# Optimization experiments

Measured on AMD Instinct MI355X. Metric: run time of the kernel, lower is better.

## Reference

```python
import jax, jax.numpy as jnp
import numpy as np

C = 128
NUM_GROUPS = 32
EPS = 1e-6


def setup_inputs() -> dict:
    key = jax.random.key(0)
    ks = jax.random.split(key, 6)
    B, H, W = 8, 64, 64
    x = jax.random.normal(ks[0], (B, C, H, W), dtype=jnp.float32)
    # 1x1 conv weights stored as [out_c, in_c] (kernel spatial dims are 1)
    fan_avg = C  # fan_in == fan_out == C for 1x1 conv
    bound = np.sqrt(3.0 / fan_avg)
    wq = jax.random.uniform(ks[1], (C, C), jnp.float32, -bound, bound)
    wk = jax.random.uniform(ks[2], (C, C), jnp.float32, -bound, bound)
    wv = jax.random.uniform(ks[3], (C, C), jnp.float32, -bound, bound)
    # proj_out has init_scale=0.0 -> near-zero init; use tiny random instead to test math
    wo = jax.random.uniform(ks[4], (C, C), jnp.float32, -bound, bound) * 1e-3
    bq = jnp.zeros((C,), jnp.float32)
    bk = jnp.zeros((C,), jnp.float32)
    bv = jnp.zeros((C,), jnp.float32)
    bo = jnp.zeros((C,), jnp.float32)
    gamma = jnp.ones((C,), jnp.float32)
    beta = jnp.zeros((C,), jnp.float32)
    return {"x": x, "gamma": gamma, "beta": beta,
            "wq": wq, "bq": bq, "wk": wk, "bk": bk,
            "wv": wv, "bv": bv, "wo": wo, "bo": bo}


def _group_norm(x, gamma, beta):
    B, Ch, H, W = x.shape
    g = NUM_GROUPS
    xg = x.reshape(B, g, Ch // g, H, W)
    mean = jnp.mean(xg, axis=(2, 3, 4), keepdims=True)
    var = jnp.var(xg, axis=(2, 3, 4), keepdims=True)
    xn = ((xg - mean) * jax.lax.rsqrt(var + EPS)).reshape(B, Ch, H, W)
    return xn * gamma[None, :, None, None] + beta[None, :, None, None]


def _conv1x1(x, w, b):
    # x: [B,C,H,W], w: [O,C], b: [O]
    return jnp.einsum('bchw,oc->bohw', x, w) + b[None, :, None, None]


def reference(x, gamma, beta, wq, bq, wk, bk, wv, bv, wo, bo):
    B, Ch, H, W = x.shape
    n = H * W
    h = _group_norm(x, gamma, beta)
    q = _conv1x1(h, wq, bq).reshape(B, Ch, n)
    k = _conv1x1(h, wk, bk).reshape(B, Ch, n)
    v = _conv1x1(h, wv, bv).reshape(B, Ch, n)
    # attn[b, i, j] = sum_c q[b,c,i] * k[b,c,j] / sqrt(C)
    attn = jnp.einsum('bci,bcj->bij', q, k) * (float(Ch) ** -0.5)
    attn = jax.nn.softmax(attn, axis=-1)
    # h[b,c,i] = sum_j v[b,c,j] * attn[b,i,j]
    out = jnp.einsum('bcj,bij->bci', v, attn).reshape(B, Ch, H, W)
    out = _conv1x1(out, wo, bo)
    return x + out
```

## Files before the change

kernel.cpp:

```cpp
#include <hip/hip_runtime.h>


typedef float f32x4 __attribute__((ext_vector_type(4)));
typedef short short8 __attribute__((ext_vector_type(8)));
typedef _Float16 half4 __attribute__((ext_vector_type(4)));
typedef unsigned short ush;
typedef unsigned short ush4 __attribute__((ext_vector_type(4)));

__device__ __forceinline__ ush f2bf(float f) {
  unsigned u = __builtin_bit_cast(unsigned, f);
  u = (u + 0x7FFFu + ((u >> 16) & 1u)) >> 16;
  return (ush)u;
}
__device__ __forceinline__ float bf2f(ush v) {
  unsigned u = ((unsigned)v) << 16;
  return __builtin_bit_cast(float, u);
}
__device__ __forceinline__ void async16(const void* g, void* l) {
  __builtin_amdgcn_global_load_lds(
      (const __attribute__((address_space(1))) unsigned int*)g,
      (__attribute__((address_space(3))) unsigned int*)l, 16, 0, 0);
}

__global__ __launch_bounds__(256) void gn_stats_kernel(
    const float* __restrict__ x, const float* __restrict__ gamma,
    const float* __restrict__ beta, float* __restrict__ scale_c,
    float* __restrict__ shift_c) {
  int bg = blockIdx.x;
  int b = bg >> 5, g = bg & 31;
  const float4* base = (const float4*)(x + (size_t)bg * 16384);
  int tid = threadIdx.x;
  float s = 0.f, sq = 0.f;
#pragma unroll
  for (int p = 0; p < 16; ++p) {
    float4 v = base[p * 256 + tid];
    s += (v.x + v.y) + (v.z + v.w);
    sq += (v.x * v.x + v.y * v.y) + (v.z * v.z + v.w * v.w);
  }
#pragma unroll
  for (int off = 32; off > 0; off >>= 1) {
    s += __shfl_down(s, off);
    sq += __shfl_down(sq, off);
  }
  __shared__ float rs[4], rq[4], mv[2];
  int w = tid >> 6, lane = tid & 63;
  if (lane == 0) { rs[w] = s; rq[w] = sq; }
  __syncthreads();
  if (tid == 0) {
    float S = (rs[0] + rs[1]) + (rs[2] + rs[3]);
    float Q = (rq[0] + rq[1]) + (rq[2] + rq[3]);
    float mean = S * (1.f / 16384.f);
    float var = Q * (1.f / 16384.f) - mean * mean;
    mv[0] = mean;
    mv[1] = rsqrtf(var + 1e-6f);
  }
  __syncthreads();
  if (tid < 4) {
    int c = (g << 2) + tid;
    float sc = mv[1] * gamma[c];
    scale_c[(b << 7) + c] = sc;
    shift_c[(b << 7) + c] = beta[c] - mv[0] * sc;
  }
}

__global__ __launch_bounds__(256) void qkv_kernel(
    const float* __restrict__ x, const float* __restrict__ scale_c,
    const float* __restrict__ shift_c, const float* __restrict__ wq,
    const float* __restrict__ wk, const float* __restrict__ wv,
    const float* __restrict__ bq, const float* __restrict__ bk,
    const float* __restrict__ bv, ush* __restrict__ Qt, ush* __restrict__ Kt,
    _Float16* __restrict__ Vh) {
  __shared__ __align__(16) ush hs[64 * 136];
  __shared__ __align__(16) ush wol[128 * 136];
  int bx = blockIdx.x;
  int type = bx >> 9;
  int rb = bx & 511;
  int b = rb >> 6, i0 = (rb & 63) << 6;
  int tid = threadIdx.x;
  int w = tid >> 6, lane = tid & 63, ln15 = lane & 15, quad = lane >> 4;

#pragma unroll
  for (int p = 0; p < 32; ++p) {
    int v = p * 256 + tid;
    int c = v >> 6, icol = v & 63;
    float xv = x[((size_t)((b << 7) + c) << 12) + i0 + icol];
    float h = xv * scale_c[(b << 7) + c] + shift_c[(b << 7) + c];
    hs[icol * 136 + c] = f2bf(h);
  }
  const float* W = type == 0 ? wq : (type == 1 ? wk : wv);
#pragma unroll
  for (int p = 0; p < 16; ++p) {
    int v = p * 256 + tid;
    int o = v >> 5, cv = (v & 31) << 2;
    float4 w4 = *(const float4*)(W + (o << 7) + cv);
    uint2 pk;
    pk.x = (unsigned)f2bf(w4.x) | ((unsigned)f2bf(w4.y) << 16);
    pk.y = (unsigned)f2bf(w4.z) | ((unsigned)f2bf(w4.w) << 16);
    *(uint2*)&wol[o * 136 + cv] = pk;
  }
  __syncthreads();

  if (type < 2) {
    f32x4 acc[8] = {};
#pragma unroll
    for (int dc = 0; dc < 4; ++dc) {
      short8 af = *(const short8*)&hs[(w * 16 + ln15) * 136 + dc * 32 + quad * 8];
#pragma unroll
      for (int nb = 0; nb < 8; ++nb) {
        short8 bf = *(const short8*)&wol[(nb * 16 + ln15) * 136 + dc * 32 + quad * 8];
        acc[nb] = __builtin_amdgcn_mfma_f32_16x16x32_bf16(af, bf, acc[nb], 0, 0, 0);
      }
    }
    const float* bias = type == 0 ? bq : bk;
    ush* dst = type == 0 ? Qt : Kt;
#pragma unroll
    for (int nb = 0; nb < 8; ++nb) {
      int o = nb * 16 + ln15;
      float bi = bias[o];
#pragma unroll
      for (int r = 0; r < 4; ++r) {
        int i = i0 + w * 16 + quad * 4 + r;
        float val = acc[nb][r] + bi;
        if (type == 0) val *= 0.08838834764831845f;
        dst[((size_t)((b << 12) + i) << 7) + o] = f2bf(val);
      }
    }
  } else {
    f32x4 acc[8] = {};
#pragma unroll
    for (int dc = 0; dc < 4; ++dc) {
      short8 bf = *(const short8*)&hs[(w * 16 + ln15) * 136 + dc * 32 + quad * 8];
#pragma unroll
      for (int mb = 0; mb < 8; ++mb) {
        short8 af = *(const short8*)&wol[(mb * 16 + ln15) * 136 + dc * 32 + quad * 8];
        acc[mb] = __builtin_amdgcn_mfma_f32_16x16x32_bf16(af, bf, acc[mb], 0, 0, 0);
      }
    }
#pragma unroll
    for (int mb = 0; mb < 8; ++mb) {
#pragma unroll
      for (int r = 0; r < 4; ++r) {
        int o = mb * 16 + quad * 4 + r;
        float val = acc[mb][r] + bv[o];
        Vh[((size_t)((b << 7) + o) << 12) + i0 + w * 16 + ln15] = (_Float16)val;
      }
    }
  }
}

__global__ __launch_bounds__(256, 2) void attn_kernel(
    const ush* __restrict__ Qt, const ush* __restrict__ Kt,
    const _Float16* __restrict__ Vh, ush* __restrict__ po,
    float* __restrict__ lw) {
  __shared__ __align__(16) ush ksb[2][4096];
  __shared__ __align__(16) _Float16 vsb[2][4096];
  int bx = blockIdx.x;
  int b = bx & 7;
  int qt = (bx >> 3) & 15;
  int ksid = bx >> 7;
  int tid = threadIdx.x;
  int w = tid >> 6, lane = tid & 63, ln15 = lane & 15, quad = lane >> 4;
  const size_t bbase = ((size_t)b) << 19;
  const size_t vbbase = ((size_t)b) << 19;
  int qbase = (qt << 8) + (w << 6);
  int j0base = ksid << 10;

  short8 qf[4][4];
#pragma unroll
  for (int ih = 0; ih < 4; ++ih)
#pragma unroll
    for (int dc = 0; dc < 4; ++dc)
      qf[ih][dc] = *(const short8*)(Qt + bbase +
          ((size_t)(qbase + ih * 16 + ln15) << 7) + dc * 32 + quad * 8);

  {
    int j0 = j0base;
#pragma unroll
    for (int c = 0; c < 2; ++c) {
      int row = w * 8 + c * 4 + (lane >> 4);
      int sg = (lane & 15) ^ (row & 15);
      async16(Kt + bbase + ((size_t)(j0 + row) << 7) + sg * 8,
              (char*)&ksb[0][0] + (w * 2 + c) * 1024);
    }
#pragma unroll
    for (int c = 0; c < 2; ++c) {
      int d = w * 32 + c * 16 + (lane >> 2);
      int sg = (lane & 3) ^ (d & 3);
      async16(Vh + vbbase + ((size_t)d << 12) + j0 + sg * 8,
              (char*)&vsb[0][0] + (w * 2 + c) * 1024);
    }
  }
  __syncthreads();

  f32x4 O[4][8] = {};
  float lsum[4] = {0.f, 0.f, 0.f, 0.f};

  for (int jt = 0; jt < 32; ++jt) {
    int buf = jt & 1;
    if (jt + 1 < 32) {
      int j0 = j0base + ((jt + 1) << 5);
      int bb = buf ^ 1;
#pragma unroll
      for (int c = 0; c < 2; ++c) {
        int row = w * 8 + c * 4 + (lane >> 4);
        int sg = (lane & 15) ^ (row & 15);
        async16(Kt + bbase + ((size_t)(j0 + row) << 7) + sg * 8,
                (char*)&ksb[bb][0] + (w * 2 + c) * 1024);
      }
#pragma unroll
      for (int c = 0; c < 2; ++c) {
        int d = w * 32 + c * 16 + (lane >> 2);
        int sg = (lane & 3) ^ (d & 3);
        async16(Vh + vbbase + ((size_t)d << 12) + j0 + sg * 8,
                (char*)&vsb[bb][0] + (w * 2 + c) * 1024);
      }
    }
    const char* kb = (const char*)&ksb[buf][0];
    const char* vb = (const char*)&vsb[buf][0];

    f32x4 S[4][2] = {};
#pragma unroll
    for (int dc = 0; dc < 4; ++dc) {
      int r0 = ln15, r1 = 16 + ln15;
      short8 kf0 = *(const short8*)(kb + r0 * 256 + (((dc * 4 + quad) ^ (r0 & 15)) << 4));
      short8 kf1 = *(const short8*)(kb + r1 * 256 + (((dc * 4 + quad) ^ (r1 & 15)) << 4));
#pragma unroll
      for (int ih = 0; ih < 4; ++ih) {
        S[ih][0] = __builtin_amdgcn_mfma_f32_16x16x32_bf16(kf0, qf[ih][dc], S[ih][0], 0, 0, 0);
        S[ih][1] = __builtin_amdgcn_mfma_f32_16x16x32_bf16(kf1, qf[ih][dc], S[ih][1], 0, 0, 0);
      }
    }
    half4 af[4][2];
#pragma unroll
    for (int ih = 0; ih < 4; ++ih) {
      float ls = 0.f;
#pragma unroll
      for (int mb = 0; mb < 2; ++mb) {
        float p0 = __expf(S[ih][mb][0] - 5.f);
        float p1 = __expf(S[ih][mb][1] - 5.f);
        float p2 = __expf(S[ih][mb][2] - 5.f);
        float p3 = __expf(S[ih][mb][3] - 5.f);
        ls += (p0 + p1) + (p2 + p3);
        half4 a;
        a.x = (_Float16)p0; a.y = (_Float16)p1;
        a.z = (_Float16)p2; a.w = (_Float16)p3;
        af[ih][mb] = a;
      }
      lsum[ih] += ls;
    }
#pragma unroll
    for (int nb = 0; nb < 8; ++nb) {
      int d = nb * 16 + ln15;
      int base = d * 64;
      int g0 = ((0 + (quad >> 1)) ^ (d & 3)) << 4;
      int g1 = ((2 + (quad >> 1)) ^ (d & 3)) << 4;
      half4 vf0 = *(const half4*)(vb + base + g0 + ((quad & 1) << 3));
      half4 vf1 = *(const half4*)(vb + base + g1 + ((quad & 1) << 3));
#pragma unroll
      for (int ih = 0; ih < 4; ++ih) {
        O[ih][nb] = __builtin_amdgcn_mfma_f32_16x16x16f16(vf0, af[ih][0], O[ih][nb], 0, 0, 0);
        O[ih][nb] = __builtin_amdgcn_mfma_f32_16x16x16f16(vf1, af[ih][1], O[ih][nb], 0, 0, 0);
      }
    }
    __syncthreads();
  }

#pragma unroll
  for (int ih = 0; ih < 4; ++ih) {
    float l = lsum[ih];
    l += __shfl_xor(l, 16);
    l += __shfl_xor(l, 32);
    if (quad == 0) lw[(ksid << 15) + (b << 12) + qbase + ih * 16 + ln15] = l;
    int i = qbase + ih * 16 + ln15;
    size_t rowb = (((size_t)((ksid * 8 + b)) << 12) + i) << 7;
#pragma unroll
    for (int nb = 0; nb < 8; ++nb) {
      ush4 pk;
      pk.x = f2bf(O[ih][nb][0]);
      pk.y = f2bf(O[ih][nb][1]);
      pk.z = f2bf(O[ih][nb][2]);
      pk.w = f2bf(O[ih][nb][3]);
      *(ush4*)(po + rowb + nb * 16 + quad * 4) = pk;
    }
  }
}

__global__ __launch_bounds__(256) void proj_kernel(
    const float* __restrict__ x, const ush* __restrict__ po,
    const float* __restrict__ lw, const float* __restrict__ wo,
    const float* __restrict__ bo, float* __restrict__ out) {
  __shared__ __align__(16) ush wol[128 * 136];
  int bx = blockIdx.x;
  int b = bx >> 6, i0 = (bx & 63) << 6;
  int tid = threadIdx.x;
  int w = tid >> 6, lane = tid & 63, ln15 = lane & 15, quad = lane >> 4;
#pragma unroll
  for (int p = 0; p < 16; ++p) {
    int v = p * 256 + tid;
    int o = v >> 5, cv = (v & 31) << 2;
    float4 w4 = *(const float4*)(wo + (o << 7) + cv);
    uint2 pk;
    pk.x = (unsigned)f2bf(w4.x) | ((unsigned)f2bf(w4.y) << 16);
    pk.y = (unsigned)f2bf(w4.z) | ((unsigned)f2bf(w4.w) << 16);
    *(uint2*)&wol[o * 136 + cv] = pk;
  }
  __syncthreads();
  int iw = i0 + w * 16;
  int i = iw + ln15;
  float rl = 0.f;
#pragma unroll
  for (int s = 0; s < 4; ++s) rl += lw[(s << 15) + (b << 12) + i];
  float rinv = 1.f / rl;

  f32x4 acc[8] = {};
#pragma unroll
  for (int dc = 0; dc < 4; ++dc) {
    float vs[8] = {0.f, 0.f, 0.f, 0.f, 0.f, 0.f, 0.f, 0.f};
#pragma unroll
    for (int s = 0; s < 4; ++s) {
      short8 pv = *(const short8*)(po + (((size_t)(s * 8 + b)) << 19) +
                                   ((size_t)i << 7) + dc * 32 + quad * 8);
#pragma unroll
      for (int e = 0; e < 8; ++e) vs[e] += bf2f((ush)pv[e]);
    }
    short8 bfv;
#pragma unroll
    for (int e = 0; e < 8; ++e) bfv[e] = (short)f2bf(vs[e] * rinv);
#pragma unroll
    for (int mb = 0; mb < 8; ++mb) {
      short8 af = *(const short8*)&wol[(mb * 16 + ln15) * 136 + dc * 32 + quad * 8];
      acc[mb] = __builtin_amdgcn_mfma_f32_16x16x32_bf16(af, bfv, acc[mb], 0, 0, 0);
    }
  }
#pragma unroll
  for (int mb = 0; mb < 8; ++mb) {
#pragma unroll
    for (int r = 0; r < 4; ++r) {
      int o = mb * 16 + quad * 4 + r;
      size_t idx = (((size_t)(b << 7) + o) << 12) + i;
      out[idx] = x[idx] + acc[mb][r] + bo[o];
    }
  }
}

extern "C" void kernel_launch(void* const* d_in, const int* in_sizes, int n_in,
                              void* d_out, int out_size, void* d_ws,
                              size_t ws_size, hipStream_t stream) {
  const float* x = (const float*)d_in[0];
  const float* gamma = (const float*)d_in[1];
  const float* beta = (const float*)d_in[2];
  const float* wq = (const float*)d_in[3];
  const float* bq = (const float*)d_in[4];
  const float* wk = (const float*)d_in[5];
  const float* bk = (const float*)d_in[6];
  const float* wv = (const float*)d_in[7];
  const float* bv = (const float*)d_in[8];
  const float* wo = (const float*)d_in[9];
  const float* bo = (const float*)d_in[10];
  float* out = (float*)d_out;

  const size_t NE = (size_t)8 * 4096 * 128;
  ush* Qt = (ush*)d_ws;
  ush* Kt = Qt + NE;
  _Float16* Vh = (_Float16*)(Kt + NE);
  ush* po = (ush*)(Vh + NE);
  float* lwp = (float*)(po + 4 * NE);
  float* scale_c = lwp + 4 * 32768;
  float* shift_c = scale_c + 1024;

  gn_stats_kernel<<<256, 256, 0, stream>>>(x, gamma, beta, scale_c, shift_c);
  qkv_kernel<<<1536, 256, 0, stream>>>(x, scale_c, shift_c, wq, wk, wv, bq, bk,
                                       bv, Qt, Kt, Vh);
  attn_kernel<<<512, 256, 0, stream>>>(Qt, Kt, Vh, po, lwp);
  proj_kernel<<<512, 256, 0, stream>>>(x, po, lwp, wo, bo, out);
}
```

Baseline: 219.0 us.

## Store Q and K in FP8 and use FP8 MFMA for attention scores

```diff
diff --git a/kernel.cpp b/kernel.cpp
--- a/kernel.cpp
+++ b/kernel.cpp
@@ -15,6 +15,25 @@
 __device__ __forceinline__ float bf2f(ush v) {
   unsigned u = ((unsigned)v) << 16;
   return __builtin_bit_cast(float, u);
+}
+__device__ __forceinline__ unsigned f2fp8(float x) {
+  unsigned u = __builtin_bit_cast(unsigned, x);
+  unsigned s = (u >> 24) & 0x80u;
+  unsigned au = u & 0x7fffffffu;
+  if (au < 0x3A800000u) return s;
+  if (au >= 0x43E00000u) return s | 0x7Eu;
+  int e = (int)(au >> 23) - 127;
+  if (e < -6) {
+    float a = __builtin_bit_cast(float, au);
+    int m = (int)(a * 512.0f + 0.5f);
+    if (m >= 8) return s | 0x08u;
+    return s | (unsigned)m;
+  }
+  unsigned keep = au >> 20, rem = au & 0xFFFFFu;
+  keep += (rem > 0x80000u) || ((rem == 0x80000u) && (keep & 1u));
+  int ef = (int)(keep >> 3) - 127;
+  if (ef >= 8 && ((ef > 8) || ((keep & 7u) == 7u))) return s | 0x7Eu;
+  return s | (unsigned)(((ef + 7) << 3) | (int)(keep & 7u));
 }
 __device__ __forceinline__ void async16(const void* g, void* l) {
   __builtin_amdgcn_global_load_lds(
@@ -68,10 +87,11 @@
     const float* __restrict__ shift_c, const float* __restrict__ wq,
     const float* __restrict__ wk, const float* __restrict__ wv,
     const float* __restrict__ bq, const float* __restrict__ bk,
-    const float* __restrict__ bv, ush* __restrict__ Qt, ush* __restrict__ Kt,
-    _Float16* __restrict__ Vh) {
+    const float* __restrict__ bv, char* __restrict__ Qt8,
+    char* __restrict__ Kt8, _Float16* __restrict__ Vh) {
   __shared__ __align__(16) ush hs[64 * 136];
   __shared__ __align__(16) ush wol[128 * 136];
+  char* hs8 = (char*)hs;
   int bx = blockIdx.x;
   int type = bx >> 9;
   int rb = bx & 511;
@@ -80,12 +100,21 @@
   int w = tid >> 6, lane = tid & 63, ln15 = lane & 15, quad = lane >> 4;
 
 #pragma unroll
-  for (int p = 0; p < 32; ++p) {
-    int v = p * 256 + tid;
-    int c = v >> 6, icol = v & 63;
-    float xv = x[((size_t)((b << 7) + c) << 12) + i0 + icol];
-    float h = xv * scale_c[(b << 7) + c] + shift_c[(b << 7) + c];
-    hs[icol * 136 + c] = f2bf(h);
+  for (int p = 0; p < 8; ++p) {
+    int id = p * 256 + tid;
+    int i = id & 63;
+    int g8 = id >> 6;
+    int c0 = g8 << 2;
+    const float* xp = x + (((size_t)((b << 7) + c0)) << 12) + i0 + i;
+    ush4 pk4;
+#pragma unroll
+    for (int e = 0; e < 4; ++e) {
+      float h = xp[(size_t)e << 12] * scale_c[(b << 7) + c0 + e] +
+                shift_c[(b << 7) + c0 + e];
+      pk4[e] = f2bf(h);
+    }
+    int pg = g8 ^ ((i & 15) << 1);
+    *(ush4*)(hs8 + i * 272 + pg * 8) = pk4;
   }
   const float* W = type == 0 ? wq : (type == 1 ? wk : wv);
 #pragma unroll
@@ -100,11 +129,15 @@
   }
   __syncthreads();
 
+#define HS_FRAG(row, dc) \
+  (*(const short8*)(hs8 + (row) * 272 + (((((dc)*4 + quad)) ^ ((row)&15)) << 4)))
+
   if (type < 2) {
     f32x4 acc[8] = {};
+    int hrow = w * 16 + ln15;
 #pragma unroll
     for (int dc = 0; dc < 4; ++dc) {
-      short8 af = *(const short8*)&hs[(w * 16 + ln15) * 136 + dc * 32 + quad * 8];
+      short8 af = HS_FRAG(hrow, dc);
 #pragma unroll
       for (int nb = 0; nb < 8; ++nb) {
         short8 bf = *(const short8*)&wol[(nb * 16 + ln15) * 136 + dc * 32 + quad * 8];
@@ -112,24 +145,32 @@
       }
     }
     const float* bias = type == 0 ? bq : bk;
-    ush* dst = type == 0 ? Qt : Kt;
+    char* dst8 = type == 0 ? Qt8 : Kt8;
+    __syncthreads();
 #pragma unroll
     for (int nb = 0; nb < 8; ++nb) {
       int o = nb * 16 + ln15;
       float bi = bias[o];
 #pragma unroll
       for (int r = 0; r < 4; ++r) {
-        int i = i0 + w * 16 + quad * 4 + r;
         float val = acc[nb][r] + bi;
         if (type == 0) val *= 0.08838834764831845f;
-        dst[((size_t)((b << 12) + i) << 7) + o] = f2bf(val);
-      }
-    }
+        hs8[(w * 16 + quad * 4 + r) * 144 + o] = (char)f2fp8(val);
+      }
+    }
+    __syncthreads();
+    int i = tid >> 2, seg = tid & 3;
+    uint4 d0 = *(const uint4*)(hs8 + i * 144 + seg * 32);
+    uint4 d1 = *(const uint4*)(hs8 + i * 144 + seg * 32 + 16);
+    char* drow = dst8 + (((size_t)((b << 12) + i0 + i)) << 7) + seg * 32;
+    *(uint4*)drow = d0;
+    *(uint4*)(drow + 16) = d1;
   } else {
     f32x4 acc[8] = {};
+    int hrow = w * 16 + ln15;
 #pragma unroll
     for (int dc = 0; dc < 4; ++dc) {
-      short8 bf = *(const short8*)&hs[(w * 16 + ln15) * 136 + dc * 32 + quad * 8];
+      short8 bf = HS_FRAG(hrow, dc);
 #pragma unroll
       for (int mb = 0; mb < 8; ++mb) {
         short8 af = *(const short8*)&wol[(mb * 16 + ln15) * 136 + dc * 32 + quad * 8];
@@ -142,17 +183,18 @@
       for (int r = 0; r < 4; ++r) {
         int o = mb * 16 + quad * 4 + r;
         float val = acc[mb][r] + bv[o];
-        Vh[((size_t)((b << 7) + o) << 12) + i0 + w * 16 + ln15] = (_Float16)val;
-      }
-    }
-  }
+        Vh[(((size_t)((b << 7) + o)) << 12) + i0 + w * 16 + ln15] = (_Float16)val;
+      }
+    }
+  }
+#undef HS_FRAG
 }
 
 __global__ __launch_bounds__(256, 2) void attn_kernel(
-    const ush* __restrict__ Qt, const ush* __restrict__ Kt,
+    const char* __restrict__ Qt8, const char* __restrict__ Kt8,
     const _Float16* __restrict__ Vh, ush* __restrict__ po,
     float* __restrict__ lw) {
-  __shared__ __align__(16) ush ksb[2][4096];
+  __shared__ __align__(16) char ksb[2][4096];
   __shared__ __align__(16) _Float16 vsb[2][4096];
   int bx = blockIdx.x;
   int b = bx & 7;
@@ -160,36 +202,40 @@
   int ksid = bx >> 7;
   int tid = threadIdx.x;
   int w = tid >> 6, lane = tid & 63, ln15 = lane & 15, quad = lane >> 4;
-  const size_t bbase = ((size_t)b) << 19;
-  const size_t vbbase = ((size_t)b) << 19;
   int qbase = (qt << 8) + (w << 6);
   int j0base = ksid << 10;
 
-  short8 qf[4][4];
-#pragma unroll
-  for (int ih = 0; ih < 4; ++ih)
+  long qf[4][4];
+#pragma unroll
+  for (int ih = 0; ih < 4; ++ih) {
+    const char* qrow =
+        Qt8 + (((size_t)((b << 12) + qbase + ih * 16 + ln15)) << 7);
 #pragma unroll
     for (int dc = 0; dc < 4; ++dc)
-      qf[ih][dc] = *(const short8*)(Qt + bbase +
-          ((size_t)(qbase + ih * 16 + ln15) << 7) + dc * 32 + quad * 8);
-
-  {
-    int j0 = j0base;
-#pragma unroll
-    for (int c = 0; c < 2; ++c) {
-      int row = w * 8 + c * 4 + (lane >> 4);
-      int sg = (lane & 15) ^ (row & 15);
-      async16(Kt + bbase + ((size_t)(j0 + row) << 7) + sg * 8,
-              (char*)&ksb[0][0] + (w * 2 + c) * 1024);
-    }
-#pragma unroll
-    for (int c = 0; c < 2; ++c) {
-      int d = w * 32 + c * 16 + (lane >> 2);
-      int sg = (lane & 3) ^ (d & 3);
-      async16(Vh + vbbase + ((size_t)d << 12) + j0 + sg * 8,
-              (char*)&vsb[0][0] + (w * 2 + c) * 1024);
-    }
-  }
+      qf[ih][dc] = *(const long*)(qrow + dc * 32 + quad * 8);
+  }
+
+  int krow = (w << 3) + (lane >> 3);
+  int ksg = (lane & 7) ^ (krow & 7);
+  const char* ksrc =
+      Kt8 + ((size_t)b << 19) + (size_t)(j0base + krow) * 128 + (ksg << 4);
+  char* kdstA = &ksb[0][0] + (w << 10);
+  char* kdstB = &ksb[1][0] + (w << 10);
+  int vsg = (lane & 3) ^ ((lane >> 4) & 3);
+  int vrow0 = (w << 5) + (lane >> 2);
+  int vrow1 = vrow0 + 16;
+  const _Float16* vsrc0 =
+      Vh + (((size_t)((b << 7) + vrow0)) << 12) + j0base + (vsg << 3);
+  const _Float16* vsrc1 =
+      Vh + (((size_t)((b << 7) + vrow1)) << 12) + j0base + (vsg << 3);
+  char* vdstA0 = (char*)&vsb[0][0] + ((w * 2 + 0) << 10);
+  char* vdstA1 = (char*)&vsb[0][0] + ((w * 2 + 1) << 10);
+  char* vdstB0 = (char*)&vsb[1][0] + ((w * 2 + 0) << 10);
+  char* vdstB1 = (char*)&vsb[1][0] + ((w * 2 + 1) << 10);
+
+  async16(ksrc, kdstA);
+  async16(vsrc0, vdstA0);
+  async16(vsrc1, vdstA1);
   __syncthreads();
 
   f32x4 O[4][8] = {};
@@ -198,36 +244,36 @@
   for (int jt = 0; jt < 32; ++jt) {
     int buf = jt & 1;
     if (jt + 1 < 32) {
-      int j0 = j0base + ((jt + 1) << 5);
-      int bb = buf ^ 1;
-#pragma unroll
-      for (int c = 0; c < 2; ++c) {
-        int row = w * 8 + c * 4 + (lane >> 4);
-        int sg = (lane & 15) ^ (row & 15);
-        async16(Kt + bbase + ((size_t)(j0 + row) << 7) + sg * 8,
-                (char*)&ksb[bb][0] + (w * 2 + c) * 1024);
-      }
-#pragma unroll
-      for (int c = 0; c < 2; ++c) {
-        int d = w * 32 + c * 16 + (lane >> 2);
-        int sg = (lane & 3) ^ (d & 3);
-        async16(Vh + vbbase + ((size_t)d << 12) + j0 + sg * 8,
-                (char*)&vsb[bb][0] + (w * 2 + c) * 1024);
-      }
-    }
-    const char* kb = (const char*)&ksb[buf][0];
+      ksrc += 4096;
+      vsrc0 += 32;
+      vsrc1 += 32;
+      if (buf == 0) {
+        async16(ksrc, kdstB);
+        async16(vsrc0, vdstB0);
+        async16(vsrc1, vdstB1);
+      } else {
+        async16(ksrc, kdstA);
+        async16(vsrc0, vdstA0);
+        async16(vsrc1, vdstA1);
+      }
+    }
+    const char* kb = &ksb[buf][0];
     const char* vb = (const char*)&vsb[buf][0];
 
     f32x4 S[4][2] = {};
 #pragma unroll
     for (int dc = 0; dc < 4; ++dc) {
       int r0 = ln15, r1 = 16 + ln15;
-      short8 kf0 = *(const short8*)(kb + r0 * 256 + (((dc * 4 + quad) ^ (r0 & 15)) << 4));
-      short8 kf1 = *(const short8*)(kb + r1 * 256 + (((dc * 4 + quad) ^ (r1 & 15)) << 4));
+      long kf0 = *(const long*)(kb + r0 * 128 +
+                                ((((dc * 2 + (quad >> 1)) ^ (r0 & 7))) << 4) +
+                                ((quad & 1) << 3));
+      long kf1 = *(const long*)(kb + r1 * 128 +
+                                ((((dc * 2 + (quad >> 1)) ^ (r1 & 7))) << 4) +
+                                ((quad & 1) << 3));
 #pragma unroll
       for (int ih = 0; ih < 4; ++ih) {
-        S[ih][0] = __builtin_amdgcn_mfma_f32_16x16x32_bf16(kf0, qf[ih][dc], S[ih][0], 0, 0, 0);
-        S[ih][1] = __builtin_amdgcn_mfma_f32_16x16x32_bf16(kf1, qf[ih][dc], S[ih][1], 0, 0, 0);
+        S[ih][0] = __builtin_amdgcn_mfma_f32_16x16x32_fp8_fp8(kf0, qf[ih][dc], S[ih][0], 0, 0, 0);
+        S[ih][1] = __builtin_amdgcn_mfma_f32_16x16x32_fp8_fp8(kf1, qf[ih][dc], S[ih][1], 0, 0, 0);
       }
     }
     half4 af[4][2];
@@ -251,11 +297,12 @@
 #pragma unroll
     for (int nb = 0; nb < 8; ++nb) {
       int d = nb * 16 + ln15;
-      int base = d * 64;
-      int g0 = ((0 + (quad >> 1)) ^ (d & 3)) << 4;
-      int g1 = ((2 + (quad >> 1)) ^ (d & 3)) << 4;
-      half4 vf0 = *(const half4*)(vb + base + g0 + ((quad & 1) << 3));
-      half4 vf1 = *(const half4*)(vb + base + g1 + ((quad & 1) << 3));
+      int sw = (ln15 >> 2) & 3;
+      const char* vrow = vb + d * 64;
+      half4 vf0 = *(const half4*)(vrow + (((0 * 2 + (quad >> 1)) ^ sw) << 4) +
+                                  ((quad & 1) << 3));
+      half4 vf1 = *(const half4*)(vrow + (((1 * 2 + (quad >> 1)) ^ sw) << 4) +
+                                  ((quad & 1) << 3));
 #pragma unroll
       for (int ih = 0; ih < 4; ++ih) {
         O[ih][nb] = __builtin_amdgcn_mfma_f32_16x16x16f16(vf0, af[ih][0], O[ih][nb], 0, 0, 0);
@@ -360,9 +407,9 @@
   float* out = (float*)d_out;
 
   const size_t NE = (size_t)8 * 4096 * 128;
-  ush* Qt = (ush*)d_ws;
-  ush* Kt = Qt + NE;
-  _Float16* Vh = (_Float16*)(Kt + NE);
+  char* Qt8 = (char*)d_ws;
+  char* Kt8 = Qt8 + NE;
+  _Float16* Vh = (_Float16*)(Kt8 + NE);
   ush* po = (ush*)(Vh + NE);
   float* lwp = (float*)(po + 4 * NE);
   float* scale_c = lwp + 4 * 32768;
@@ -370,7 +417,7 @@
 
   gn_stats_kernel<<<256, 256, 0, stream>>>(x, gamma, beta, scale_c, shift_c);
   qkv_kernel<<<1536, 256, 0, stream>>>(x, scale_c, shift_c, wq, wk, wv, bq, bk,
-                                       bv, Qt, Kt, Vh);
-  attn_kernel<<<512, 256, 0, stream>>>(Qt, Kt, Vh, po, lwp);
+                                       bv, Qt8, Kt8, Vh);
+  attn_kernel<<<512, 256, 0, stream>>>(Qt8, Kt8, Vh, po, lwp);
   proj_kernel<<<512, 256, 0, stream>>>(x, po, lwp, wo, bo, out);
 }
```

New measurement: 204.7 us. -6.6%, faster.
